# Kernel optimization log

Hardware: AMD Instinct MI355X
Metric: run time of the kernel (lower is better)

Reference implementation:

```python
import jax, jax.numpy as jnp
import numpy as np

FS = 16000.0
SOUND_SPEED = 343.0
MAX_ORDER = 10
FILTER_LEN = 81            # fractional-delay sinc filter taps (torchaudio default)
PAD = FILTER_LEN // 2      # 40
RIR_LEN = 8000             # static RIR length; bounds max delay for 10 m rooms, order 10

# ---- static image-source lattice: all (i,j,k) with |i|+|j|+|k| <= MAX_ORDER ----
_ind = np.arange(-MAX_ORDER, MAX_ORDER + 1)
_g = np.stack(np.meshgrid(_ind, _ind, _ind, indexing="ij"), -1).reshape(-1, 3)
_g = _g[np.abs(_g).sum(-1) <= MAX_ORDER]                      # (n_img=1561, 3)
XYZ = jnp.asarray(_g, dtype=jnp.float32)                      # (n_img, 3)
EXP_LO = jnp.asarray(np.abs(np.floor(_g / 2.0)), jnp.float32)        # reflections off x=0/y=0/z=0 walls
EXP_HI = jnp.asarray(np.abs(np.floor((_g + 1) / 2.0)), jnp.float32)  # reflections off far walls
ODD = jnp.asarray(_g % 2 == 1)                                # (n_img, 3) bool


def _hann(x, T):
    # truncated Hann window used by the fractional-delay filter
    return jnp.where(jnp.abs(x) <= T / 2, 0.5 * (1.0 + jnp.cos(2.0 * jnp.pi * x / T)), 0.0)


def _rir_one(room, mic, src, absorption):
    # room, mic, src: (3,) metres; absorption: (6,) per-wall absorption coeff
    # image-source positions: mirror source across walls per parity of lattice index
    img = jnp.where(ODD, room * (XYZ + 1.0) - src, room * XYZ + src)   # (n_img, 3)
    tr = jnp.sqrt(1.0 - absorption)                                     # wall reflection coeffs (6,)
    att = jnp.prod((tr[::2] ** EXP_LO) * (tr[1::2] ** EXP_HI), axis=-1)  # (n_img,)
    dist = jnp.linalg.norm(img - mic, axis=-1)                           # (n_img,)
    amp = att / dist                                                     # 1/r spreading
    delay = dist * FS / SOUND_SPEED                                      # delay in samples (float)
    delay_i = jnp.ceil(delay)                                            # integer anchor
    n = jnp.arange(-PAD, PAD + 1, dtype=jnp.float32)                     # (81,)
    x = n[None, :] + delay_i[:, None] - delay[:, None]                   # (n_img, 81)
    irs = amp[:, None] * jnp.sinc(x) * _hann(x, 2 * PAD)                 # windowed-sinc frac delay
    # scatter-add each 81-tap filter at offset delay_i - PAD into the RIR buffer
    idx = delay_i.astype(jnp.int32)[:, None] - PAD + jnp.arange(FILTER_LEN, dtype=jnp.int32)
    valid = (idx >= 0) & (idx < RIR_LEN)
    rir = jnp.zeros((RIR_LEN,), irs.dtype).at[jnp.clip(idx, 0, RIR_LEN - 1)].add(
        jnp.where(valid, irs, 0.0))
    return rir


def setup_inputs() -> dict:
    key = jax.random.key(0)
    k1, k2, k3, k4 = jax.random.split(key, 4)
    B = 256
    room = 3.0 + 7.0 * jax.random.uniform(k1, (B, 3), jnp.float32)       # room dims in [3,10] m
    mic_f = 0.05 + 0.40 * jax.random.uniform(k2, (B, 3), jnp.float32)    # mic frac in [0.05,0.45]
    src_f = 0.55 + 0.40 * jax.random.uniform(k3, (B, 3), jnp.float32)    # src frac in [0.55,0.95]
    absorp = 0.1 + 0.4 * jax.random.uniform(k4, (B, 1), jnp.float32)     # absorption in [0.1,0.5]
    inp = jnp.concatenate([room, mic_f, src_f, absorp], axis=1)          # (B, 10)
    return {"input": inp}


def reference(input):
    room = input[:, 0:3]
    mic = input[:, 3:6] * room
    src = input[:, 6:9] * room
    absorption = jnp.repeat(input[:, 9:10], 6, axis=1)                   # uniform over 6 walls
    rir = jax.vmap(_rir_one)(room, mic, src, absorption)                 # (B, RIR_LEN)
    dist = jnp.linalg.norm(mic - src, axis=1)
    toa = 40.0 + FS * dist / SOUND_SPEED                                 # (B,)
    return rir, toa
```

## Files before the change

### kernel.cpp

```cpp
#include <hip/hip_runtime.h>
#include <math.h>

#define NB 256
#define NIMG 1561
#define RIRLEN 8000
#define PADI 40
#define NTHREADS 1024
#define NBKT 505
#define NSTARTP 512
#define NPAIR 63

struct ImgTab { unsigned int v[NIMG]; };

constexpr ImgTab build_tab() {
    ImgTab t{};
    int n = 0;
    for (int x = -10; x <= 10; ++x)
        for (int y = -10; y <= 10; ++y)
            for (int z = -10; z <= 10; ++z) {
                int ax = x < 0 ? -x : x;
                int ay = y < 0 ? -y : y;
                int az = z < 0 ? -z : z;
                int l1 = ax + ay + az;
                if (l1 <= 10) {
                    t.v[n++] = (unsigned)(x + 10) | ((unsigned)(y + 10) << 5) |
                               ((unsigned)(z + 10) << 10) | ((unsigned)l1 << 15);
                }
            }
    return t;
}

constexpr int tab_count() {
    int n = 0;
    for (int x = -10; x <= 10; ++x)
        for (int y = -10; y <= 10; ++y)
            for (int z = -10; z <= 10; ++z) {
                int ax = x < 0 ? -x : x;
                int ay = y < 0 ? -y : y;
                int az = z < 0 ? -z : z;
                if (ax + ay + az <= 10) ++n;
            }
    return n;
}
static_assert(tab_count() == NIMG, "image count mismatch");

__constant__ ImgTab c_tab = build_tab();

__global__ __launch_bounds__(NTHREADS) void
rir_kernel(const float* __restrict__ in, float* __restrict__ out) {
    __shared__ float4 s_rec[NIMG + 1];
    __shared__ float  s_trpow[11];
    __shared__ int    s_hist[NBKT];
    __shared__ int    s_scan[512];
    __shared__ int    s_start[NSTARTP];
    __shared__ int    s_cursor[NBKT];
    __shared__ int    s_nspike;
    __shared__ int    s_spike_idx[64];
    __shared__ float  s_spike_amp[64];

    const int b   = blockIdx.x;
    const int tid = threadIdx.x;
    const float* p = in + b * 10;

    if (tid < NBKT) s_hist[tid] = 0;
    if (tid == 0) {
        float tr = sqrtf(1.0f - p[9]);
        float pw = 1.0f;
        for (int k = 0; k <= 10; ++k) { s_trpow[k] = pw; pw *= tr; }
        s_nspike = 0;
        s_rec[NIMG] = make_float4(0.0f, 0.0f, 0.0f, -1.0e6f);
    }
    __syncthreads();

    const float rx = p[0], ry = p[1], rz = p[2];
    const float mx = p[3] * rx, my = p[4] * ry, mz = p[5] * rz;
    const float sx = p[6] * rx, sy = p[7] * ry, sz = p[8] * rz;
    const float K = 16000.0f / 343.0f;
    const float INV_PI = 0.31830988618379067154f;

    float4 rec[2];
    int ibkt[2]  = {0, 0};
    bool ivalid[2] = {false, false};

    for (int u = 0; u < 2; ++u) {
        int i = tid + u * NTHREADS;
        if (i < NIMG) {
            unsigned v = c_tab.v[i];
            int gx = (int)(v & 31u) - 10;
            int gy = (int)((v >> 5) & 31u) - 10;
            int gz = (int)((v >> 10) & 31u) - 10;
            int l1 = (int)(v >> 15);

            float ix = (gx & 1) ? rx * (float)(gx + 1) - sx : rx * (float)gx + sx;
            float iy = (gy & 1) ? ry * (float)(gy + 1) - sy : ry * (float)gy + sy;
            float iz = (gz & 1) ? rz * (float)(gz + 1) - sz : rz * (float)gz + sz;

            float dx = ix - mx, dy = iy - my, dz = iz - mz;
            float dist = sqrtf(dx * dx + dy * dy + dz * dz);

            float amp  = s_trpow[l1] / dist;
            float d    = dist * K;
            float dlc  = ceilf(d);
            float frac = dlc - d;
            int   idlc = (int)dlc;
            int   base = idlc - PADI;

            if (base < RIRLEN) {
                if (frac == 0.0f) {
                    if (idlc < RIRLEN) {
                        int sp = atomicAdd(&s_nspike, 1);
                        if (sp < 64) { s_spike_idx[sp] = idlc; s_spike_amp[sp] = amp; }
                    }
                } else {
                    float spf = (frac < 1.0e-3f) ? frac : (sinpif(frac) * INV_PI);
                    float S   = amp * spf;
                    if (idlc & 1) S = -S;
                    float hS  = 0.5f * S;
                    float cd  = cospif(d * 0.025f);
                    float sd  = sinpif(d * 0.025f);
                    rec[u] = make_float4(hS, hS * cd, hS * sd, d);
                    ibkt[u]   = (base + 80) >> 4;
                    ivalid[u] = true;
                    atomicAdd(&s_hist[ibkt[u]], 1);
                }
            }
        }
    }
    __syncthreads();

    if (tid < 512) s_scan[tid] = (tid < NBKT) ? s_hist[tid] : 0;
    __syncthreads();
    for (int d = 1; d < 512; d <<= 1) {
        int y = 0;
        if (tid < 512 && tid >= d) y = s_scan[tid - d];
        __syncthreads();
        if (tid < 512) s_scan[tid] += y;
        __syncthreads();
    }
    if (tid < NBKT) {
        s_start[tid + 1] = s_scan[tid];
        s_cursor[tid]    = (tid == 0) ? 0 : s_scan[tid - 1];
        if (tid == 0) s_start[0] = 0;
    }
    if (tid >= NBKT + 1 && tid < NSTARTP) s_start[tid] = s_scan[NBKT - 1];
    __syncthreads();

    for (int u = 0; u < 2; ++u) {
        if (ivalid[u]) {
            int pos = atomicAdd(&s_cursor[ibkt[u]], 1);
            s_rec[pos] = rec[u];
        }
    }
    __syncthreads();

    const int wave = tid >> 6;
    const int lane = tid & 63;
    const int h    = lane >> 5;
    const int l5   = lane & 31;
    float* __restrict__ ob = out + (size_t)b * RIRLEN;

    for (int q = wave; q < NPAIR; q += NTHREADS / 64) {
        const int s  = 2 * q + h;
        const int n0 = (q << 7) + (h << 6) + l5;
        const int n1 = n0 + 32;
        const float fn0 = (float)n0, fn1 = (float)n1;
        const float cn0 = cospif(fn0 * 0.025f), sn0 = sinpif(fn0 * 0.025f);
        const float cn1 = cospif(fn1 * 0.025f), sn1 = sinpif(fn1 * 0.025f);

        const int lo = s_start[4 * s];
        const int hi = s_start[4 * s + 9];
        int lenA = __shfl(hi - lo, 0);
        int lenB = __shfl(hi - lo, 32);
        const int trips = (lenA > lenB) ? lenA : lenB;

        float acc0 = 0.0f, acc1 = 0.0f;
        int k = lo;
#pragma clang loop unroll_count(4)
        for (int it = 0; it < trips; ++it, ++k) {
            int kc = (k < hi) ? k : NIMG;
            float4 r = s_rec[kc];
            float x0 = fn0 - r.w;
            float x1 = fn1 - r.w;
            float t0 = fmaf(r.y, cn0, r.x); t0 = fmaf(r.z, sn0, t0);
            float t1 = fmaf(r.y, cn1, r.x); t1 = fmaf(r.z, sn1, t1);
            t0 = (fabsf(x0) < 40.0f) ? t0 : 0.0f;
            t1 = (fabsf(x1) < 40.0f) ? t1 : 0.0f;
            acc0 = fmaf(t0, __builtin_amdgcn_rcpf(x0), acc0);
            acc1 = fmaf(t1, __builtin_amdgcn_rcpf(x1), acc1);
        }
        const float sgn = (n0 & 1) ? -1.0f : 1.0f;
        if (n0 < RIRLEN) ob[n0] = acc0 * sgn;
        if (n1 < RIRLEN) ob[n1] = acc1 * sgn;
    }

    __syncthreads();
    int nsp = s_nspike; nsp = (nsp < 64) ? nsp : 64;
    if (tid < nsp) atomicAdd(&ob[s_spike_idx[tid]], s_spike_amp[tid]);

    if (tid == 0) {
        float dx = mx - sx, dy = my - sy, dz = mz - sz;
        out[(size_t)NB * RIRLEN + b] = 40.0f + sqrtf(dx * dx + dy * dy + dz * dz) * K;
    }
}

extern "C" void kernel_launch(void* const* d_in, const int* in_sizes, int n_in,
                              void* d_out, int out_size, void* d_ws, size_t ws_size,
                              hipStream_t stream) {
    const float* in = (const float*)d_in[0];
    float* out = (float*)d_out;
    rir_kernel<<<dim3(NB), dim3(NTHREADS), 0, stream>>>(in, out);
}
```

Baseline: 83.49 us.

## Add dynamic wave work-stealing and trim per-tap math in RIR synthesis loop

Replaces the static round-robin assignment of output chunks to waves with a shared-memory atomic counter so waves grab the next chunk dynamically. The inner loop is split into a bounds-check-free main part up to the shorter half-wave's length and a guarded tail. Per-tap work is reduced by deriving the second sample's phase from the first with a fixed rotation, and by masking the window through an infinite denominator instead of selecting the numerator. Unroll goes from 4 to 8. The aim is less load imbalance and fewer ALU ops per tap, at the cost of one LDS atomic plus a shuffle per chunk.

```diff
diff --git a/kernel.cpp b/kernel.cpp
--- a/kernel.cpp
+++ b/kernel.cpp
@@ -6,6 +6,7 @@
 #define RIRLEN 8000
 #define PADI 40
 #define NTHREADS 1024
+#define NWAVES (NTHREADS / 64)
 #define NBKT 505
 #define NSTARTP 512
 #define NPAIR 63
@@ -54,6 +55,7 @@
     __shared__ int    s_scan[512];
     __shared__ int    s_start[NSTARTP];
     __shared__ int    s_cursor[NBKT];
+    __shared__ int    s_qnext;
     __shared__ int    s_nspike;
     __shared__ int    s_spike_idx[64];
     __shared__ float  s_spike_amp[64];
@@ -68,6 +70,7 @@
         float pw = 1.0f;
         for (int k = 0; k <= 10; ++k) { s_trpow[k] = pw; pw *= tr; }
         s_nspike = 0;
+        s_qnext  = NWAVES;
         s_rec[NIMG] = make_float4(0.0f, 0.0f, 0.0f, -1.0e6f);
     }
     __syncthreads();
@@ -157,40 +160,63 @@
     const int lane = tid & 63;
     const int h    = lane >> 5;
     const int l5   = lane & 31;
+    const float sgn  = (l5 & 1) ? -1.0f : 1.0f;
+    const float vinf = __builtin_inff();
     float* __restrict__ ob = out + (size_t)b * RIRLEN;
 
-    for (int q = wave; q < NPAIR; q += NTHREADS / 64) {
-        const int s  = 2 * q + h;
+    int q = wave;
+    while (q < NPAIR) {
         const int n0 = (q << 7) + (h << 6) + l5;
         const int n1 = n0 + 32;
-        const float fn0 = (float)n0, fn1 = (float)n1;
+        const float fn0 = (float)n0;
         const float cn0 = cospif(fn0 * 0.025f), sn0 = sinpif(fn0 * 0.025f);
-        const float cn1 = cospif(fn1 * 0.025f), sn1 = sinpif(fn1 * 0.025f);
-
-        const int lo = s_start[4 * s];
-        const int hi = s_start[4 * s + 9];
-        int lenA = __shfl(hi - lo, 0);
-        int lenB = __shfl(hi - lo, 32);
-        const int trips = (lenA > lenB) ? lenA : lenB;
+        const float cn1 = -sn0, sn1 = cn0;
+        const float c32 = cospif(0.8f), s32 = sinpif(0.8f);
+        const float cnn1 = cn0 * c32 - sn0 * s32;
+        const float snn1 = sn0 * c32 + cn0 * s32;
+        (void)cn1; (void)sn1;
+
+        const int loA = s_start[8 * q];
+        const int hiA = s_start[8 * q + 9];
+        const int loB = s_start[8 * q + 4];
+        const int hiB = s_start[8 * q + 13];
+        const int lenA = hiA - loA, lenB = hiB - loB;
+        const int lmin = (lenA < lenB) ? lenA : lenB;
+        const int lmax = (lenA > lenB) ? lenA : lenB;
+        const int lo   = h ? loB : loA;
+        const int hi   = h ? hiB : hiA;
 
         float acc0 = 0.0f, acc1 = 0.0f;
-        int k = lo;
-#pragma clang loop unroll_count(4)
-        for (int it = 0; it < trips; ++it, ++k) {
-            int kc = (k < hi) ? k : NIMG;
-            float4 r = s_rec[kc];
+#pragma clang loop unroll_count(8)
+        for (int it = 0; it < lmin; ++it) {
+            float4 r = s_rec[lo + it];
             float x0 = fn0 - r.w;
-            float x1 = fn1 - r.w;
-            float t0 = fmaf(r.y, cn0, r.x); t0 = fmaf(r.z, sn0, t0);
-            float t1 = fmaf(r.y, cn1, r.x); t1 = fmaf(r.z, sn1, t1);
-            t0 = (fabsf(x0) < 40.0f) ? t0 : 0.0f;
-            t1 = (fabsf(x1) < 40.0f) ? t1 : 0.0f;
-            acc0 = fmaf(t0, __builtin_amdgcn_rcpf(x0), acc0);
-            acc1 = fmaf(t1, __builtin_amdgcn_rcpf(x1), acc1);
-        }
-        const float sgn = (n0 & 1) ? -1.0f : 1.0f;
+            float x1 = x0 + 32.0f;
+            float xm0 = (fabsf(x0) < 40.0f) ? x0 : vinf;
+            float xm1 = (fabsf(x1) < 40.0f) ? x1 : vinf;
+            float t0 = fmaf(r.y, cn0, r.x);  t0 = fmaf(r.z, sn0, t0);
+            float t1 = fmaf(r.y, cnn1, r.x); t1 = fmaf(r.z, snn1, t1);
+            acc0 = fmaf(t0, __builtin_amdgcn_rcpf(xm0), acc0);
+            acc1 = fmaf(t1, __builtin_amdgcn_rcpf(xm1), acc1);
+        }
+        for (int it = lmin; it < lmax; ++it) {
+            int k = lo + it;
+            float4 r = s_rec[(k < hi) ? k : NIMG];
+            float x0 = fn0 - r.w;
+            float x1 = x0 + 32.0f;
+            float xm0 = (fabsf(x0) < 40.0f) ? x0 : vinf;
+            float xm1 = (fabsf(x1) < 40.0f) ? x1 : vinf;
+            float t0 = fmaf(r.y, cn0, r.x);  t0 = fmaf(r.z, sn0, t0);
+            float t1 = fmaf(r.y, cnn1, r.x); t1 = fmaf(r.z, snn1, t1);
+            acc0 = fmaf(t0, __builtin_amdgcn_rcpf(xm0), acc0);
+            acc1 = fmaf(t1, __builtin_amdgcn_rcpf(xm1), acc1);
+        }
         if (n0 < RIRLEN) ob[n0] = acc0 * sgn;
         if (n1 < RIRLEN) ob[n1] = acc1 * sgn;
+
+        int nq;
+        if (lane == 0) nq = atomicAdd(&s_qnext, 1);
+        q = __shfl(nq, 0);
     }
 
     __syncthreads();
```

Result: faster. 80.67 us (-3.4%).
